# Kernel tuning notes

Hardware: AMD Instinct MI355X
Metric: run time of the kernel (lower is better)

Reference implementation:

```python
import jax, jax.numpy as jnp
import numpy as np

K = 30          # hard-coded in Hypergraph.from_feature_kNN(ft, k=30)
BN_EPS = 1e-5   # BatchNorm1d eval mode, running_mean=0, running_var=1


def setup_inputs() -> dict:
    key = jax.random.key(0)
    ks = jax.random.split(key, 3)
    B, C, H, W = 8, 64, 56, 56
    hid = 32
    return {
        "x": jax.random.normal(ks[0], (B, C, H, W), jnp.float32),
        "w1": jax.random.normal(ks[1], (C, hid), jnp.float32) / np.sqrt(C).astype(np.float32),
        "b1": jnp.zeros((hid,), jnp.float32),
        "g1": jnp.ones((hid,), jnp.float32),
        "be1": jnp.zeros((hid,), jnp.float32),
        "w2": jax.random.normal(ks[2], (hid, C), jnp.float32) / np.sqrt(hid).astype(np.float32),
        "b2": jnp.zeros((C,), jnp.float32),
        "g2": jnp.ones((C,), jnp.float32),
        "be2": jnp.zeros((C,), jnp.float32),
    }


def _knn_idx(ft, k):
    # squared euclidean distances via gram trick; same ordering as torch.cdist
    sq = jnp.sum(ft * ft, axis=1)
    d2 = sq[:, None] + sq[None, :] - 2.0 * (ft @ ft.T)   # [L, L]
    _, idx = jax.lax.top_k(-d2, k)                        # k smallest distances (incl. self)
    return idx                                            # [L, k] -> hyperedge e = kNN of vertex e


def _v2v_mean(X, nbr):
    # hg.v2v(X, aggr="mean"): v2e mean then e2v mean over the kNN incidence structure
    L, k = nbr.shape
    F = X.shape[1]
    Y = jnp.mean(X[nbr], axis=1)                                        # v2e: [L_edges, F]
    seg = nbr.reshape(-1)                                               # vertex nbr[e,j] belongs to edge e
    vals = jnp.broadcast_to(Y[:, None, :], (L, k, F)).reshape(L * k, F)
    s = jax.ops.segment_sum(vals, seg, num_segments=L)                  # e2v sum
    dv = jax.ops.segment_sum(jnp.ones((L * k,), X.dtype), seg, num_segments=L)
    return s / jnp.maximum(dv, 1.0)[:, None]                            # e2v mean


def _bn_eval(x, g, b):
    # BatchNorm1d in eval: running_mean=0, running_var=1
    return x * (g * np.float32(1.0 / np.sqrt(1.0 + BN_EPS))) + b


def reference(x, w1, b1, g1, be1, w2, b2, g2, be2):
    B, C, H, W = x.shape
    L = H * W
    xf = x.reshape(B, L, C)  # faithful raw x.view(B, L, C) (no transpose in source)

    def per_sample(ft):
        nbr = _knn_idx(ft, K)
        # HGNNPConv 1: theta -> bn -> v2v(mean) -> relu (dropout off in eval)
        h = _bn_eval(ft @ w1 + b1, g1, be1)
        h = jax.nn.relu(_v2v_mean(h, nbr))
        # HGNNPConv 2 (is_last): theta -> bn -> v2v(mean), no act/drop
        h = _bn_eval(h @ w2 + b2, g2, be2)
        return _v2v_mean(h, nbr)  # [L, C]

    outs = jax.vmap(per_sample)(xf)      # [B, L, C]
    return outs.reshape(B, -1, H, W)     # faithful raw outs.view(B, -1, H, W)
```

## Files before the change

### kernel.cpp

```cpp
#include <hip/hip_runtime.h>
#include <math.h>


namespace {

constexpr int cB = 8;
constexpr int cL = 3136;
constexpr int cC = 64;
constexpr int cH = 32;
constexpr int cK = 30;
constexpr int NV = cB * cL;
constexpr int QD = 10;
constexpr float BN_SC = 0.99999500003749964f;

typedef __bf16 bf16x8 __attribute__((ext_vector_type(8)));
typedef float floatx4 __attribute__((ext_vector_type(4)));

union BU {
  __bf16 b[2];
  unsigned u;
};

__device__ inline unsigned umin2(unsigned a, unsigned b) { return a < b ? a : b; }
__device__ inline unsigned umax2(unsigned a, unsigned b) { return a > b ? a : b; }
__device__ inline unsigned umin3(unsigned a, unsigned b, unsigned c) {
  return umin2(umin2(a, b), c);
}
__device__ inline float bf16lo(unsigned u) { return __uint_as_float(u << 16); }
__device__ inline float bf16hi(unsigned u) {
  return __uint_as_float(u & 0xFFFF0000u);
}

__device__ inline unsigned bclean64(unsigned v, int ln) {
#pragma unroll
  for (int off = 32; off; off >>= 1) {
    unsigned p = (unsigned)__shfl_xor((int)v, off);
    v = (ln & off) ? umax2(v, p) : umin2(v, p);
  }
  return v;
}

__global__ __launch_bounds__(256) void k_splitth(
    const float* __restrict__ x, const float* __restrict__ w1,
    const float* __restrict__ b1, const float* __restrict__ g1,
    const float* __restrict__ be1, ushort* __restrict__ xhi,
    ushort* __restrict__ xlo, float* __restrict__ sqf,
    int* __restrict__ cnt, int* __restrict__ cur, __bf16* __restrict__ h1) {
  __shared__ float w1s[cC * cH];
  __shared__ float xs[8 * 64];
  const int t = threadIdx.x;
  const int v0 = blockIdx.x * 8;
  for (int n = t; n < cC * cH; n += 256) w1s[n] = w1[n];
  {
    float2 xv = reinterpret_cast<const float2*>(x + (size_t)v0 * 64)[t];
    xs[2 * t] = xv.x;
    xs[2 * t + 1] = xv.y;
    BU hh, ll;
    hh.b[0] = (__bf16)xv.x;
    hh.b[1] = (__bf16)xv.y;
    ll.b[0] = (__bf16)(xv.x - (float)hh.b[0]);
    ll.b[1] = (__bf16)(xv.y - (float)hh.b[1]);
    reinterpret_cast<unsigned*>(xhi)[(size_t)v0 * 32 + t] = hh.u;
    reinterpret_cast<unsigned*>(xlo)[(size_t)v0 * 32 + t] = ll.u;
    float ss = xv.x * xv.x + xv.y * xv.y;
#pragma unroll
    for (int off = 1; off < 32; off <<= 1) ss += __shfl_xor(ss, off);
    if ((t & 31) == 0) sqf[v0 + (t >> 5)] = ss * 1024.f + 262144.f;
  }
  if (t < 8) {
    cnt[v0 + t] = 0;
    cur[v0 + t] = 0;
  }
  __syncthreads();
  const int r = t >> 5, f = t & 31;
  float s = 0.f;
#pragma unroll
  for (int k = 0; k < cC; ++k) s = fmaf(xs[r * 64 + k], w1s[k * cH + f], s);
  h1[(size_t)(v0 + r) * cH + f] =
      (__bf16)((s + b1[f]) * (g1[f] * BN_SC) + be1[f]);
}

__global__ __launch_bounds__(64, 4) void k_sweep(
    const ushort* __restrict__ xhi, const ushort* __restrict__ xlo,
    const float* __restrict__ sqf, unsigned* __restrict__ candq) {
  const int ib = blockIdx.x, qt = blockIdx.y, b = blockIdx.z;
  const int r0 = ib * 16;
  const int jb0 = qt * 1568;
  const size_t bbase = (size_t)b * cL;
  const int ln = threadIdx.x;
  const int tx = ln & 15;
  const int qd = ln >> 4;

  const size_t aoff = (bbase + r0 + tx) * 64 + qd * 8;
  const bf16x8 aH0 = *reinterpret_cast<const bf16x8*>(&xhi[aoff]);
  const bf16x8 aH1 = *reinterpret_cast<const bf16x8*>(&xhi[aoff + 32]);
  const bf16x8 aL0 = *reinterpret_cast<const bf16x8*>(&xlo[aoff]);
  const bf16x8 aL1 = *reinterpret_cast<const bf16x8*>(&xlo[aoff + 32]);

  unsigned q[4][QD];
#pragma unroll
  for (int e = 0; e < 4; ++e)
#pragma unroll
    for (int k = 0; k < QD; ++k) q[e][k] = 0xFFFFFFFFu;

  const ushort* ph0 = xhi + (bbase + jb0 + tx) * 64 + qd * 8;
  const ushort* ph1 = ph0 + 16 * 64;
  const ushort* pl0 = xlo + (bbase + jb0 + tx) * 64 + qd * 8;
  const ushort* pl1 = pl0 + 16 * 64;
  const float* ps = sqf + bbase + jb0 + tx;

  for (int st = 0; st < 49; ++st) {
    bf16x8 b0h0 = *reinterpret_cast<const bf16x8*>(ph0);
    bf16x8 b0h1 = *reinterpret_cast<const bf16x8*>(ph0 + 32);
    bf16x8 b0l0 = *reinterpret_cast<const bf16x8*>(pl0);
    bf16x8 b0l1 = *reinterpret_cast<const bf16x8*>(pl0 + 32);
    bf16x8 b1h0 = *reinterpret_cast<const bf16x8*>(ph1);
    bf16x8 b1h1 = *reinterpret_cast<const bf16x8*>(ph1 + 32);
    bf16x8 b1l0 = *reinterpret_cast<const bf16x8*>(pl1);
    bf16x8 b1l1 = *reinterpret_cast<const bf16x8*>(pl1 + 32);
    const float sj0 = ps[0];
    const float sj1 = ps[16];

    floatx4 acc0 = {0.f, 0.f, 0.f, 0.f};
    acc0 = __builtin_amdgcn_mfma_f32_16x16x32_bf16(aH0, b0h0, acc0, 0, 0, 0);
    acc0 = __builtin_amdgcn_mfma_f32_16x16x32_bf16(aH1, b0h1, acc0, 0, 0, 0);
    acc0 = __builtin_amdgcn_mfma_f32_16x16x32_bf16(aH0, b0l0, acc0, 0, 0, 0);
    acc0 = __builtin_amdgcn_mfma_f32_16x16x32_bf16(aH1, b0l1, acc0, 0, 0, 0);
    acc0 = __builtin_amdgcn_mfma_f32_16x16x32_bf16(aL0, b0h0, acc0, 0, 0, 0);
    acc0 = __builtin_amdgcn_mfma_f32_16x16x32_bf16(aL1, b0h1, acc0, 0, 0, 0);
    floatx4 acc1 = {0.f, 0.f, 0.f, 0.f};
    acc1 = __builtin_amdgcn_mfma_f32_16x16x32_bf16(aH0, b1h0, acc1, 0, 0, 0);
    acc1 = __builtin_amdgcn_mfma_f32_16x16x32_bf16(aH1, b1h1, acc1, 0, 0, 0);
    acc1 = __builtin_amdgcn_mfma_f32_16x16x32_bf16(aH0, b1l0, acc1, 0, 0, 0);
    acc1 = __builtin_amdgcn_mfma_f32_16x16x32_bf16(aH1, b1l1, acc1, 0, 0, 0);
    acc1 = __builtin_amdgcn_mfma_f32_16x16x32_bf16(aL0, b1h0, acc1, 0, 0, 0);
    acc1 = __builtin_amdgcn_mfma_f32_16x16x32_bf16(aL1, b1h1, acc1, 0, 0, 0);

    const unsigned col0 = (unsigned)(jb0 + st * 32 + tx);
    unsigned pk0[4], pk1[4];
#pragma unroll
    for (int e = 0; e < 4; ++e) {
      float q0 = fmaf(acc0[e], -2048.f, sj0);
      q0 = fminf(fmaxf(q0, 0.f), 1048575.f);
      pk0[e] = ((unsigned)q0 << 12) | col0;
      float q1 = fmaf(acc1[e], -2048.f, sj1);
      q1 = fminf(fmaxf(q1, 0.f), 1048575.f);
      pk1[e] = ((unsigned)q1 << 12) | (col0 + 16);
    }

#pragma unroll
    for (int e = 0; e < 4; ++e) {
      unsigned a0 = umin2(pk0[e], pk1[e]);
      unsigned a1 = umax2(pk0[e], pk1[e]);
#pragma unroll
      for (int i = QD - 1; i >= 2; --i)
        q[e][i] = umin3(q[e][i], umax2(q[e][i - 1], a0),
                        umax2(q[e][i - 2], a1));
      q[e][1] = umin3(q[e][1], umax2(q[e][0], a0), a1);
      q[e][0] = umin3(q[e][0], a0, a1);
    }

    ph0 += 2048; ph1 += 2048; pl0 += 2048; pl1 += 2048; ps += 32;
  }

  unsigned* cr[4];
#pragma unroll
  for (int e = 0; e < 4; ++e)
    cr[e] = candq + (bbase + r0 + qd * 4 + e) * 80 + qt * 40;
  for (int it = 0; it < 40; ++it) {
    unsigned h0 = q[0][0], h1 = q[1][0], h2 = q[2][0], h3 = q[3][0];
    unsigned m0 = h0, m1 = h1, m2 = h2, m3 = h3;
#pragma unroll
    for (int off = 1; off < 16; off <<= 1) {
      m0 = umin2(m0, (unsigned)__shfl_xor((int)m0, off));
      m1 = umin2(m1, (unsigned)__shfl_xor((int)m1, off));
      m2 = umin2(m2, (unsigned)__shfl_xor((int)m2, off));
      m3 = umin2(m3, (unsigned)__shfl_xor((int)m3, off));
    }
    if (tx == 0) {
      cr[0][it] = m0;
      cr[1][it] = m1;
      cr[2][it] = m2;
      cr[3][it] = m3;
    }
    if (h0 == m0) {
#pragma unroll
      for (int k = 0; k < QD - 1; ++k) q[0][k] = q[0][k + 1];
      q[0][QD - 1] = 0xFFFFFFFFu;
    }
    if (h1 == m1) {
#pragma unroll
      for (int k = 0; k < QD - 1; ++k) q[1][k] = q[1][k + 1];
      q[1][QD - 1] = 0xFFFFFFFFu;
    }
    if (h2 == m2) {
#pragma unroll
      for (int k = 0; k < QD - 1; ++k) q[2][k] = q[2][k + 1];
      q[2][QD - 1] = 0xFFFFFFFFu;
    }
    if (h3 == m3) {
#pragma unroll
      for (int k = 0; k < QD - 1; ++k) q[3][k] = q[3][k + 1];
      q[3][QD - 1] = 0xFFFFFFFFu;
    }
  }
}

__global__ __launch_bounds__(256) void k_rescore(
    const float* __restrict__ x, const unsigned* __restrict__ candq,
    const __bf16* __restrict__ h1, int* __restrict__ nbr,
    int* __restrict__ cnt, __bf16* __restrict__ Y1) {
  const int w  = threadIdx.x >> 6;
  const int ln = threadIdx.x & 63;
  const size_t row = (size_t)blockIdx.x * 4 + w;
  const size_t bvert = row - (row % cL);

  const unsigned* cq = candq + row * 80;
  unsigned A = (ln < 40) ? cq[ln]      : 0xFFFFFFFFu;
  unsigned B = (ln < 40) ? cq[40 + ln] : 0xFFFFFFFFu;

  unsigned g = umin2(A, (unsigned)__shfl((int)B, 63 - ln));
  g = bclean64(g, ln);

  const unsigned qv = g >> 12;
  const int col = min((int)(g & 0xFFFu), cL - 1);

  unsigned q29 = (unsigned)__shfl((int)qv, 29);
  unsigned q30 = (unsigned)__shfl((int)qv, 30);
  int myc = col;
  if (!(q30 > q29 + 6)) {
    float4 xi[16];
    const float4* xi4 = reinterpret_cast<const float4*>(x + row * 64);
#pragma unroll
    for (int c = 0; c < 16; ++c) xi[c] = xi4[c];
    double dv = 1e300;
    if (ln < 40) {
      const float4* xj4 =
          reinterpret_cast<const float4*>(x + (bvert + col) * 64);
      double ax = 0.0, ay = 0.0, az = 0.0, aw = 0.0;
#pragma unroll
      for (int c = 0; c < 16; ++c) {
        float4 xj = xj4[c];
        double d0 = (double)xi[c].x - (double)xj.x; ax = fma(d0, d0, ax);
        double d1 = (double)xi[c].y - (double)xj.y; ay = fma(d1, d1, ay);
        double d2 = (double)xi[c].z - (double)xj.z; az = fma(d2, d2, az);
        double d3 = (double)xi[c].w - (double)xj.w; aw = fma(d3, d3, aw);
      }
      dv = (ax + ay) + (az + aw);
    }
    int r2 = 0;
    for (int j = 0; j < 40; ++j) {
      double od = __shfl(dv, j);
      r2 += (od < dv || (od == dv && j < ln)) ? 1 : 0;
    }
    myc = __builtin_amdgcn_ds_permute(r2 << 2, col);
  }
  if (ln < cK) {
    nbr[row * cK + ln] = myc;
    atomicAdd(&cnt[bvert + myc], 1);
  }

  const unsigned* Xb = reinterpret_cast<const unsigned*>(h1 + bvert * cH);
  const int qg = ln >> 4, f2 = ln & 15;
  float s0 = 0.f, s1 = 0.f;
#pragma unroll
  for (int m = 0; m < 8; ++m) {
    int j = m * 4 + qg;
    int idx = __shfl(myc, j < cK ? j : 0);
    unsigned u = Xb[(size_t)idx * 16 + f2];
    bool ok = j < cK;
    s0 += ok ? bf16lo(u) : 0.f;
    s1 += ok ? bf16hi(u) : 0.f;
  }
  s0 += __shfl_xor(s0, 16);
  s1 += __shfl_xor(s1, 16);
  s0 += __shfl_xor(s0, 32);
  s1 += __shfl_xor(s1, 32);
  if (ln < 16) {
    BU cv;
    cv.b[0] = (__bf16)(s0 * (1.f / 30.f));
    cv.b[1] = (__bf16)(s1 * (1.f / 30.f));
    reinterpret_cast<unsigned*>(Y1)[row * 16 + f2] = cv.u;
  }
}

__global__ __launch_bounds__(1024) void k_scan(const int* __restrict__ cnt,
                                               int* __restrict__ rp) {
  const int b = blockIdx.x;
  const int* c = cnt + b * cL;
  int* r = rp + b * (cL + 1);
  const int t = threadIdx.x;
  const int ln = t & 63, w = t >> 6;

  int v[4];
  int s = 0;
#pragma unroll
  for (int i = 0; i < 4; ++i) {
    int idx = 4 * t + i;
    v[i] = (idx < cL) ? c[idx] : 0;
    s += v[i];
  }
  int inc = s;
#pragma unroll
  for (int off = 1; off < 64; off <<= 1) {
    int u = __shfl_up(inc, off);
    if (ln >= off) inc += u;
  }
  __shared__ int wsum[16];
  if (ln == 63) wsum[w] = inc;
  __syncthreads();
  int carry = 0;
#pragma unroll
  for (int i = 0; i < 16; ++i) carry += (i < w) ? wsum[i] : 0;

  int excl = carry + inc - s;
#pragma unroll
  for (int i = 0; i < 4; ++i) {
    int idx = 4 * t + i;
    if (idx < cL) r[idx] = excl;
    excl += v[i];
  }
  if (t == 1023) r[cL] = excl;
}

__global__ void k_fill(const int* __restrict__ nbr, const int* __restrict__ rp,
                       int* __restrict__ cur, int* __restrict__ el) {
  int g = blockIdx.x * 256 + threadIdx.x;
  if (g >= NV * cK) return;
  int b = g / (cL * cK);
  int e = (g / cK) % cL;
  int v = nbr[g];
  v = min(max(v, 0), cL - 1);
  int p = rp[b * (cL + 1) + v] + atomicAdd(&cur[b * cL + v], 1);
  p = min(max(p, 0), cL * cK - 1);
  el[(size_t)b * cL * cK + p] = e;
}

__global__ __launch_bounds__(256) void k_e2v_t2(const __bf16* __restrict__ Y,
                                                const int* __restrict__ rp,
                                                const int* __restrict__ el,
                                                const float* __restrict__ w2,
                                                const float* __restrict__ b2,
                                                const float* __restrict__ g2,
                                                const float* __restrict__ be2,
                                                __bf16* __restrict__ h2) {
  __shared__ float w2s[cH * cC];
  {
    int t = threadIdx.x;
    for (int n = t; n < cH * cC; n += 256) w2s[n] = w2[n];
  }
  const int w  = threadIdx.x >> 6;
  const int ln = threadIdx.x & 63;
  const size_t vr = (size_t)blockIdx.x * 4 + w;
  const size_t b  = vr / cL;
  const int v = (int)(vr % cL);
  const int* rpb = rp + b * (cL + 1);
  const int s0 = rpb[v];
  const int deg = rpb[v + 1] - s0;
  const int* elb = el + b * (size_t)cL * cK + s0;
  const __bf16* Yb = Y + b * cL * cH;
  const int hi = ln >> 5, f = ln & 31;
  float s = 0.f;

  for (int base = 0; base < deg; base += 64) {
    const int take = min(64, deg - base);
    const int eidx = elb[base + (ln < take ? ln : 0)];
    for (int j0 = 0; j0 < take; j0 += 16) {
      float acc = 0.f;
#pragma unroll
      for (int k2 = 0; k2 < 8; ++k2) {
        int j = j0 + 2 * k2 + hi;
        int e0 = __shfl(eidx, j < take ? j : 0);
        float y = (float)Yb[(size_t)e0 * cH + f];
        acc += (j < take) ? y : 0.f;
      }
      s += acc;
    }
  }
  __syncthreads();

  s += __shfl_xor(s, 32);
  float r = fmaxf(s / (float)deg, 0.f);

  float s2 = 0.f;
#pragma unroll 8
  for (int k = 0; k < cH; ++k) {
    float rk = __shfl(r, k);
    s2 = fmaf(rk, w2s[k * cC + ln], s2);
  }
  h2[vr * cC + ln] = (__bf16)((s2 + b2[ln]) * (g2[ln] * BN_SC) + be2[ln]);
}

__global__ __launch_bounds__(256) void k_v2e64(const __bf16* __restrict__ X,
                                               const int* __restrict__ nbr,
                                               __bf16* __restrict__ Y) {
  const int w  = threadIdx.x >> 6;
  const int ln = threadIdx.x & 63;
  const size_t er = (size_t)blockIdx.x * 4 + w;
  const size_t b  = er / cL;
  const unsigned* Xb = reinterpret_cast<const unsigned*>(X + b * cL * cC);
  const int nb_l = nbr[er * cK + (ln < cK ? ln : cK - 1)];
  const int half = ln >> 5, f2 = ln & 31;
  int idx[15];
#pragma unroll
  for (int m = 0; m < 15; ++m) idx[m] = __shfl(nb_l, 2 * m + half);
  unsigned v[15];
#pragma unroll
  for (int m = 0; m < 15; ++m) v[m] = Xb[(size_t)idx[m] * 32 + f2];
  float s0 = 0.f, s1 = 0.f;
#pragma unroll
  for (int m = 0; m < 15; ++m) {
    s0 += bf16lo(v[m]);
    s1 += bf16hi(v[m]);
  }
  s0 += __shfl_xor(s0, 32);
  s1 += __shfl_xor(s1, 32);
  if (half == 0) {
    BU cv;
    cv.b[0] = (__bf16)(s0 * (1.f / 30.f));
    cv.b[1] = (__bf16)(s1 * (1.f / 30.f));
    reinterpret_cast<unsigned*>(Y)[er * 32 + f2] = cv.u;
  }
}

__global__ __launch_bounds__(256) void k_e2v64(const __bf16* __restrict__ Y,
                                               const int* __restrict__ rp,
                                               const int* __restrict__ el,
                                               float* __restrict__ out) {
  const int w  = threadIdx.x >> 6;
  const int ln = threadIdx.x & 63;
  const size_t vr = (size_t)blockIdx.x * 4 + w;
  const size_t b  = vr / cL;
  const int v = (int)(vr % cL);
  const int* rpb = rp + b * (cL + 1);
  const int s0r = rpb[v];
  const int deg = rpb[v + 1] - s0r;
  const int* elb = el + b * (size_t)cL * cK + s0r;
  const unsigned* Yb = reinterpret_cast<const unsigned*>(Y + b * cL * cC);
  const int half = ln >> 5, f2 = ln & 31;
  float s0 = 0.f, s1 = 0.f;

  for (int base = 0; base < deg; base += 64) {
    const int take = min(64, deg - base);
    const int eidx = elb[base + (ln < take ? ln : 0)];
    for (int j0 = 0; j0 < take; j0 += 16) {
      float a0 = 0.f, a1 = 0.f;
#pragma unroll
      for (int k2 = 0; k2 < 8; ++k2) {
        int j = j0 + 2 * k2 + half;
        int e0 = __shfl(eidx, j < take ? j : 0);
        unsigned u = Yb[(size_t)e0 * 32 + f2];
        bool ok = j < take;
        a0 += ok ? bf16lo(u) : 0.f;
        a1 += ok ? bf16hi(u) : 0.f;
      }
      s0 += a0;
      s1 += a1;
    }
  }
  s0 += __shfl_xor(s0, 32);
  s1 += __shfl_xor(s1, 32);
  float v0 = __shfl(s0, ln >> 1);
  float v1 = __shfl(s1, ln >> 1);
  out[vr * cC + ln] = ((ln & 1) ? v1 : v0) / (float)deg;
}

}

extern "C" void kernel_launch(void* const* d_in, const int* in_sizes, int n_in,
                              void* d_out, int out_size, void* d_ws,
                              size_t ws_size, hipStream_t stream) {
  (void)in_sizes; (void)n_in; (void)out_size; (void)ws_size;
  const float* x   = (const float*)d_in[0];
  const float* w1  = (const float*)d_in[1];
  const float* b1  = (const float*)d_in[2];
  const float* g1  = (const float*)d_in[3];
  const float* be1 = (const float*)d_in[4];
  const float* w2  = (const float*)d_in[5];
  const float* b2  = (const float*)d_in[6];
  const float* g2  = (const float*)d_in[7];
  const float* be2 = (const float*)d_in[8];
  float* out = (float*)d_out;

  char* base = (char*)d_ws;
  size_t off = 0;
  auto carve = [&](size_t bytes) {
    char* p = base + off;
    off += (bytes + 255) & ~(size_t)255;
    return p;
  };
  float* sqf = (float*)carve((size_t)NV * 4);
  int*   nbr = (int*)carve((size_t)NV * cK * 4);
  int*   rp  = (int*)carve((size_t)cB * (cL + 1) * 4);
  int*   cnt = (int*)carve((size_t)NV * 4);
  int*   cur = (int*)carve((size_t)NV * 4);
  char* RA = carve((size_t)NV * 64 * 2 * 2);
  ushort* xhi = (ushort*)RA;
  ushort* xlo = (ushort*)(RA + 3211264);
  int* el = (int*)RA;
  char* RC = carve(17661952);
  unsigned* candq = (unsigned*)RC;
  __bf16* h1 = (__bf16*)(RC + 8028160);
  __bf16* Y1 = (__bf16*)(RC + 9633792);
  __bf16* h2 = (__bf16*)(RC + 11239424);
  __bf16* Y2 = (__bf16*)(RC + 14450688);

  k_splitth<<<NV / 8, 256, 0, stream>>>(x, w1, b1, g1, be1, xhi, xlo, sqf,
                                        cnt, cur, h1);
  k_sweep<<<dim3(196, 2, cB), 64, 0, stream>>>(xhi, xlo, sqf, candq);
  k_rescore<<<NV / 4, 256, 0, stream>>>(x, candq, h1, nbr, cnt, Y1);

  k_scan<<<cB, 1024, 0, stream>>>(cnt, rp);
  k_fill<<<(NV * cK) / 256, 256, 0, stream>>>(nbr, rp, cur, el);

  k_e2v_t2<<<NV / 4, 256, 0, stream>>>(Y1, rp, el, w2, b2, g2, be2, h2);
  k_v2e64<<<NV / 4, 256, 0, stream>>>(h2, nbr, Y2);
  k_e2v64<<<NV / 4, 256, 0, stream>>>(Y2, rp, el, out);
}
```

Measured before the change: 437.1 us.

## Stage kNN column tiles in shared memory shared by two waves with register prefetch

```diff
diff --git a/kernel.cpp b/kernel.cpp
--- a/kernel.cpp
+++ b/kernel.cpp
@@ -80,22 +80,44 @@
       (__bf16)((s + b1[f]) * (g1[f] * BN_SC) + be1[f]);
 }
 
-__global__ __launch_bounds__(64, 4) void k_sweep(
+__global__ __launch_bounds__(128, 4) void k_sweep(
     const ushort* __restrict__ xhi, const ushort* __restrict__ xlo,
     const float* __restrict__ sqf, unsigned* __restrict__ candq) {
   const int ib = blockIdx.x, qt = blockIdx.y, b = blockIdx.z;
-  const int r0 = ib * 16;
+  const int r0 = ib * 32;
   const int jb0 = qt * 1568;
+  const int ntile = 49;
   const size_t bbase = (size_t)b * cL;
-  const int ln = threadIdx.x;
+
+  __shared__ ushort aHi[32 * 72], aLo[32 * 72];
+  __shared__ ushort bHi[32 * 72], bLo[32 * 72];
+  __shared__ float sqJs[32];
+
+  const int t  = threadIdx.x;
+  const int ln = t & 63;
+  const int w  = t >> 6;
   const int tx = ln & 15;
   const int qd = ln >> 4;
 
-  const size_t aoff = (bbase + r0 + tx) * 64 + qd * 8;
-  const bf16x8 aH0 = *reinterpret_cast<const bf16x8*>(&xhi[aoff]);
-  const bf16x8 aH1 = *reinterpret_cast<const bf16x8*>(&xhi[aoff + 32]);
-  const bf16x8 aL0 = *reinterpret_cast<const bf16x8*>(&xlo[aoff]);
-  const bf16x8 aL1 = *reinterpret_cast<const bf16x8*>(&xlo[aoff + 32]);
+#pragma unroll
+  for (int it = 0; it < 2; ++it) {
+    int idx = t + 128 * it;
+    int r = idx >> 3, blk = idx & 7;
+    *reinterpret_cast<uint4*>(&aHi[r * 72 + blk * 8]) =
+        *reinterpret_cast<const uint4*>(&xhi[(bbase + r0 + r) * 64 + blk * 8]);
+    *reinterpret_cast<uint4*>(&aLo[r * 72 + blk * 8]) =
+        *reinterpret_cast<const uint4*>(&xlo[(bbase + r0 + r) * 64 + blk * 8]);
+  }
+  __syncthreads();
+
+  bf16x8 aH[2], aL[2];
+#pragma unroll
+  for (int kk = 0; kk < 2; ++kk) {
+    aH[kk] = *reinterpret_cast<const bf16x8*>(
+        &aHi[(w * 16 + tx) * 72 + kk * 32 + qd * 8]);
+    aL[kk] = *reinterpret_cast<const bf16x8*>(
+        &aLo[(w * 16 + tx) * 72 + kk * 32 + qd * 8]);
+  }
 
   unsigned q[4][QD];
 #pragma unroll
@@ -103,55 +125,67 @@
 #pragma unroll
     for (int k = 0; k < QD; ++k) q[e][k] = 0xFFFFFFFFu;
 
-  const ushort* ph0 = xhi + (bbase + jb0 + tx) * 64 + qd * 8;
-  const ushort* ph1 = ph0 + 16 * 64;
-  const ushort* pl0 = xlo + (bbase + jb0 + tx) * 64 + qd * 8;
-  const ushort* pl1 = pl0 + 16 * 64;
-  const float* ps = sqf + bbase + jb0 + tx;
-
-  for (int st = 0; st < 49; ++st) {
-    bf16x8 b0h0 = *reinterpret_cast<const bf16x8*>(ph0);
-    bf16x8 b0h1 = *reinterpret_cast<const bf16x8*>(ph0 + 32);
-    bf16x8 b0l0 = *reinterpret_cast<const bf16x8*>(pl0);
-    bf16x8 b0l1 = *reinterpret_cast<const bf16x8*>(pl0 + 32);
-    bf16x8 b1h0 = *reinterpret_cast<const bf16x8*>(ph1);
-    bf16x8 b1h1 = *reinterpret_cast<const bf16x8*>(ph1 + 32);
-    bf16x8 b1l0 = *reinterpret_cast<const bf16x8*>(pl1);
-    bf16x8 b1l1 = *reinterpret_cast<const bf16x8*>(pl1 + 32);
-    const float sj0 = ps[0];
-    const float sj1 = ps[16];
-
-    floatx4 acc0 = {0.f, 0.f, 0.f, 0.f};
-    acc0 = __builtin_amdgcn_mfma_f32_16x16x32_bf16(aH0, b0h0, acc0, 0, 0, 0);
-    acc0 = __builtin_amdgcn_mfma_f32_16x16x32_bf16(aH1, b0h1, acc0, 0, 0, 0);
-    acc0 = __builtin_amdgcn_mfma_f32_16x16x32_bf16(aH0, b0l0, acc0, 0, 0, 0);
-    acc0 = __builtin_amdgcn_mfma_f32_16x16x32_bf16(aH1, b0l1, acc0, 0, 0, 0);
-    acc0 = __builtin_amdgcn_mfma_f32_16x16x32_bf16(aL0, b0h0, acc0, 0, 0, 0);
-    acc0 = __builtin_amdgcn_mfma_f32_16x16x32_bf16(aL1, b0h1, acc0, 0, 0, 0);
-    floatx4 acc1 = {0.f, 0.f, 0.f, 0.f};
-    acc1 = __builtin_amdgcn_mfma_f32_16x16x32_bf16(aH0, b1h0, acc1, 0, 0, 0);
-    acc1 = __builtin_amdgcn_mfma_f32_16x16x32_bf16(aH1, b1h1, acc1, 0, 0, 0);
-    acc1 = __builtin_amdgcn_mfma_f32_16x16x32_bf16(aH0, b1l0, acc1, 0, 0, 0);
-    acc1 = __builtin_amdgcn_mfma_f32_16x16x32_bf16(aH1, b1l1, acc1, 0, 0, 0);
-    acc1 = __builtin_amdgcn_mfma_f32_16x16x32_bf16(aL0, b1h0, acc1, 0, 0, 0);
-    acc1 = __builtin_amdgcn_mfma_f32_16x16x32_bf16(aL1, b1h1, acc1, 0, 0, 0);
-
-    const unsigned col0 = (unsigned)(jb0 + st * 32 + tx);
-    unsigned pk0[4], pk1[4];
+  const int pr  = (t + 0)   >> 3, pblk  = (t + 0)   & 7;
+  const int pr1 = (t + 128) >> 3, pblk1 = (t + 128) & 7;
+  uint4 pH0, pH1, pL0, pL1;
+  float pS = 0.f;
+  {
+    const int jb = jb0;
+    pH0 = *reinterpret_cast<const uint4*>(&xhi[(bbase + jb + pr) * 64 + pblk * 8]);
+    pL0 = *reinterpret_cast<const uint4*>(&xlo[(bbase + jb + pr) * 64 + pblk * 8]);
+    pH1 = *reinterpret_cast<const uint4*>(&xhi[(bbase + jb + pr1) * 64 + pblk1 * 8]);
+    pL1 = *reinterpret_cast<const uint4*>(&xlo[(bbase + jb + pr1) * 64 + pblk1 * 8]);
+    if (t < 32) pS = sqf[bbase + jb + t];
+  }
+
+  for (int st = 0; st < ntile; ++st) {
+    __syncthreads();
+    *reinterpret_cast<uint4*>(&bHi[pr * 72 + pblk * 8])   = pH0;
+    *reinterpret_cast<uint4*>(&bLo[pr * 72 + pblk * 8])   = pL0;
+    *reinterpret_cast<uint4*>(&bHi[pr1 * 72 + pblk1 * 8]) = pH1;
+    *reinterpret_cast<uint4*>(&bLo[pr1 * 72 + pblk1 * 8]) = pL1;
+    if (t < 32) sqJs[t] = pS;
+    __syncthreads();
+
+    if (st + 1 < ntile) {
+      const int jb = jb0 + (st + 1) * 32;
+      pH0 = *reinterpret_cast<const uint4*>(&xhi[(bbase + jb + pr) * 64 + pblk * 8]);
+      pL0 = *reinterpret_cast<const uint4*>(&xlo[(bbase + jb + pr) * 64 + pblk * 8]);
+      pH1 = *reinterpret_cast<const uint4*>(&xhi[(bbase + jb + pr1) * 64 + pblk1 * 8]);
+      pL1 = *reinterpret_cast<const uint4*>(&xlo[(bbase + jb + pr1) * 64 + pblk1 * 8]);
+      if (t < 32) pS = sqf[bbase + jb + t];
+    }
+    __builtin_amdgcn_sched_barrier(0);
+
+    unsigned pk[2][4];
+#pragma unroll
+    for (int f = 0; f < 2; ++f) {
+      const int bro = (f * 16 + tx) * 72 + qd * 8;
+      bf16x8 bh0 = *reinterpret_cast<const bf16x8*>(&bHi[bro]);
+      bf16x8 bh1 = *reinterpret_cast<const bf16x8*>(&bHi[bro + 32]);
+      bf16x8 bl0 = *reinterpret_cast<const bf16x8*>(&bLo[bro]);
+      bf16x8 bl1 = *reinterpret_cast<const bf16x8*>(&bLo[bro + 32]);
+      floatx4 acc = {0.f, 0.f, 0.f, 0.f};
+      acc = __builtin_amdgcn_mfma_f32_16x16x32_bf16(aH[0], bh0, acc, 0, 0, 0);
+      acc = __builtin_amdgcn_mfma_f32_16x16x32_bf16(aH[1], bh1, acc, 0, 0, 0);
+      acc = __builtin_amdgcn_mfma_f32_16x16x32_bf16(aH[0], bl0, acc, 0, 0, 0);
+      acc = __builtin_amdgcn_mfma_f32_16x16x32_bf16(aH[1], bl1, acc, 0, 0, 0);
+      acc = __builtin_amdgcn_mfma_f32_16x16x32_bf16(aL[0], bh0, acc, 0, 0, 0);
+      acc = __builtin_amdgcn_mfma_f32_16x16x32_bf16(aL[1], bh1, acc, 0, 0, 0);
+      const float sjs = sqJs[f * 16 + tx];
+      const unsigned col = (unsigned)(jb0 + st * 32 + f * 16 + tx);
+#pragma unroll
+      for (int e = 0; e < 4; ++e) {
+        float qf = fmaf(acc[e], -2048.f, sjs);
+        qf = fminf(fmaxf(qf, 0.f), 1048575.f);
+        pk[f][e] = ((unsigned)qf << 12) | col;
+      }
+    }
+
 #pragma unroll
     for (int e = 0; e < 4; ++e) {
-      float q0 = fmaf(acc0[e], -2048.f, sj0);
-      q0 = fminf(fmaxf(q0, 0.f), 1048575.f);
-      pk0[e] = ((unsigned)q0 << 12) | col0;
-      float q1 = fmaf(acc1[e], -2048.f, sj1);
-      q1 = fminf(fmaxf(q1, 0.f), 1048575.f);
-      pk1[e] = ((unsigned)q1 << 12) | (col0 + 16);
-    }
-
-#pragma unroll
-    for (int e = 0; e < 4; ++e) {
-      unsigned a0 = umin2(pk0[e], pk1[e]);
-      unsigned a1 = umax2(pk0[e], pk1[e]);
+      unsigned a0 = umin2(pk[0][e], pk[1][e]);
+      unsigned a1 = umax2(pk[0][e], pk[1][e]);
 #pragma unroll
       for (int i = QD - 1; i >= 2; --i)
         q[e][i] = umin3(q[e][i], umax2(q[e][i - 1], a0),
@@ -159,14 +193,12 @@
       q[e][1] = umin3(q[e][1], umax2(q[e][0], a0), a1);
       q[e][0] = umin3(q[e][0], a0, a1);
     }
-
-    ph0 += 2048; ph1 += 2048; pl0 += 2048; pl1 += 2048; ps += 32;
   }
 
   unsigned* cr[4];
 #pragma unroll
   for (int e = 0; e < 4; ++e)
-    cr[e] = candq + (bbase + r0 + qd * 4 + e) * 80 + qt * 40;
+    cr[e] = candq + (bbase + r0 + w * 16 + qd * 4 + e) * 80 + qt * 40;
   for (int it = 0; it < 40; ++it) {
     unsigned h0 = q[0][0], h1 = q[1][0], h2 = q[2][0], h3 = q[3][0];
     unsigned m0 = h0, m1 = h1, m2 = h2, m3 = h3;
@@ -507,7 +539,7 @@
 
   k_splitth<<<NV / 8, 256, 0, stream>>>(x, w1, b1, g1, be1, xhi, xlo, sqf,
                                         cnt, cur, h1);
-  k_sweep<<<dim3(196, 2, cB), 64, 0, stream>>>(xhi, xlo, sqf, candq);
+  k_sweep<<<dim3(98, 2, cB), 128, 0, stream>>>(xhi, xlo, sqf, candq);
   k_rescore<<<NV / 4, 256, 0, stream>>>(x, candq, h1, nbr, cnt, Y1);
 
   k_scan<<<cB, 1024, 0, stream>>>(cnt, rp);
```

Result: faster. 373.5 us (-14.5%).
